# Optimization experiments

Measured on AMD Instinct MI355X. Metric: run time of the kernel, lower is better.

Reference implementation:

```python
import jax, jax.numpy as jnp
import numpy as np

H = 16
D = 64
EPS = 1e-6

def _phi(x):
    # elu_feature_map: elu(x) + 1
    return jax.nn.elu(x) + 1.0

def setup_inputs() -> dict:
    key = jax.random.key(0)
    k1, k2, k3, k4 = jax.random.split(key, 4)
    B, N = 4, 4096
    query = jax.random.normal(k1, (B, N, H * D), dtype=jnp.float32)
    key_t = jax.random.normal(k2, (B, N, H * D), dtype=jnp.float32)
    value = jax.random.normal(k3, (B, N, H * D), dtype=jnp.float32)
    W_out = jax.random.normal(k4, (D, H * D), dtype=jnp.float32) * (1.0 / np.sqrt(H * D))
    b_out = jnp.zeros((D,), dtype=jnp.float32)
    return {"query": query, "key": key_t, "value": value, "W_out": W_out, "b_out": b_out}

def reference(query, key, value, W_out, b_out):
    B, N, _ = query.shape
    # b n (h d) -> b h n d
    def split_heads(x):
        return x.reshape(B, N, H, D).transpose(0, 2, 1, 3)
    q = split_heads(query)
    k = split_heads(key)
    v = split_heads(value)
    Q = _phi(q)  # [B,H,N,D]
    K = _phi(k)
    # KV aggregation: O(N D^2)
    KV = jnp.einsum('bhnd,bhnm->bhdm', K, v)          # [B,H,D,D]
    Ksum = K.sum(axis=2)                               # [B,H,D]
    Z = 1.0 / (jnp.einsum('bhnd,bhd->bhn', Q, Ksum) + EPS)  # [B,H,N]
    out = jnp.einsum('bhnd,bhdm,bhn->bhnm', Q, KV, Z)  # [B,H,N,D]
    # b h n d -> b n h d -> (b*n, h*d)
    out = out.transpose(0, 2, 1, 3).reshape(B * N, H * D)
    return out @ W_out.T + b_out
```

## Files before the change

### kernel.cpp

```cpp
#include <hip/hip_runtime.h>

#define B_  4
#define N_  4096
#define H_  16
#define BH_ 64
#define S_  16
#define ST_ 72
#define EPS_ 1e-6f

#define NST_ 40
#define WTILE_ (64 * NST_)
#define WPOOL_ (2 * WTILE_)

typedef _Float16 h2  __attribute__((ext_vector_type(2)));
typedef _Float16 h8  __attribute__((ext_vector_type(8)));
typedef float    f4v __attribute__((ext_vector_type(4)));

struct H2x2 { h2 a, b; };
struct H2x4 { h2 e[4]; };

__device__ __forceinline__ h8 ld_h8(const _Float16* p) {
    f4v r = *(const f4v*)p;
    return __builtin_bit_cast(h8, r);
}
__device__ __forceinline__ H2x4 ld_h2x4(const _Float16* p) {
    f4v r = *(const f4v*)p;
    return __builtin_bit_cast(H2x4, r);
}
__device__ __forceinline__ void st_h2x2(_Float16* p, h2 a, h2 b) {
    H2x2 t{a, b};
    *(float2*)p = __builtin_bit_cast(float2, t);
}
__device__ __forceinline__ float phi(float x) {
    return x > 0.0f ? x + 1.0f : __expf(x);
}
__device__ __forceinline__ float fdot2(h2 a, h2 b, float c) {
    return __builtin_amdgcn_fdot2(a, b, c, false);
}
__device__ __forceinline__ f4v gload(const void* p) {
    f4v r;
    asm volatile("global_load_dwordx4 %0, %1, off"
                 : "=v"(r) : "v"(p) : "memory");
    return r;
}
#define VMW(N)                                                    \
    do {                                                          \
        asm volatile("s_waitcnt vmcnt(" #N ")" ::: "memory");     \
        __builtin_amdgcn_sched_barrier(0);                        \
    } while (0)

__global__ __launch_bounds__(256, 2) void k_kvpart(const float* __restrict__ K,
                                                   const float* __restrict__ V,
                                                   float* __restrict__ kvpart,
                                                   float* __restrict__ kspart) {
    const int s = blockIdx.x, h4 = blockIdx.y, b = blockIdx.z;
    const int t = threadIdx.x, wv = t >> 6, lane = t & 63;
    const int rp = lane >> 4, c4 = lane & 15;
    const int h = h4 * 4 + wv;

    __shared__ __align__(16) _Float16 pool[4 * WPOOL_];

    _Float16* Kt = pool + wv * WPOOL_;
    _Float16* Vt = Kt + WTILE_;

    f4v kr[8], vr[8];
    const float* baseK = K + ((size_t)(b * N_ + s * 256) * 1024 + h * 64 + c4 * 4);
    const float* baseV = V + ((size_t)(b * N_ + s * 256) * 1024 + h * 64 + c4 * 4);

    auto LOADX = [&](int chunk) {
        const int ro = (chunk * 32 + 8 * rp) * 1024;
        const float* gk = baseK + ro;
        const float* gv = baseV + ro;
#pragma unroll
        for (int r = 0; r < 8; ++r) kr[r] = gload(gk + r * 1024);
#pragma unroll
        for (int r = 0; r < 8; ++r) vr[r] = gload(gv + r * 1024);
    };
    auto STOREX = [&]() {
        const int nn = 8 * rp;
#pragma unroll
        for (int dj = 0; dj < 4; ++dj) {
            const int d = 4 * c4 + dj;
            h2 lo, hi;
            lo.x = (_Float16)phi(kr[0][dj]); lo.y = (_Float16)phi(kr[1][dj]);
            hi.x = (_Float16)phi(kr[2][dj]); hi.y = (_Float16)phi(kr[3][dj]);
            st_h2x2(&Kt[d * NST_ + nn], lo, hi);
            lo.x = (_Float16)phi(kr[4][dj]); lo.y = (_Float16)phi(kr[5][dj]);
            hi.x = (_Float16)phi(kr[6][dj]); hi.y = (_Float16)phi(kr[7][dj]);
            st_h2x2(&Kt[d * NST_ + nn + 4], lo, hi);
            lo.x = (_Float16)vr[0][dj]; lo.y = (_Float16)vr[1][dj];
            hi.x = (_Float16)vr[2][dj]; hi.y = (_Float16)vr[3][dj];
            st_h2x2(&Vt[d * NST_ + nn], lo, hi);
            lo.x = (_Float16)vr[4][dj]; lo.y = (_Float16)vr[5][dj];
            hi.x = (_Float16)vr[6][dj]; hi.y = (_Float16)vr[7][dj];
            st_h2x2(&Vt[d * NST_ + nn + 4], lo, hi);
        }
    };

    f4v acc[4][4];
#pragma unroll
    for (int i = 0; i < 4; ++i)
#pragma unroll
        for (int j = 0; j < 4; ++j) acc[i][j] = (f4v){0.f, 0.f, 0.f, 0.f};
    float ksum = 0.f;
    h2 one2; one2.x = (_Float16)1.0f; one2.y = (_Float16)1.0f;

    const int fo = rp * 8;

    auto COMPUTE = [&]() {
        h8 af[4], bf[4];
#pragma unroll
        for (int i = 0; i < 4; ++i) {
            af[i] = ld_h8(&Kt[(16 * i + c4) * NST_ + fo]);
            bf[i] = ld_h8(&Vt[(16 * i + c4) * NST_ + fo]);
        }
#pragma unroll
        for (int i = 0; i < 4; ++i)
#pragma unroll
            for (int j = 0; j < 4; ++j)
                acc[i][j] = __builtin_amdgcn_mfma_f32_16x16x32_f16(af[i], bf[j], acc[i][j], 0, 0, 0);
#pragma unroll
        for (int q = 0; q < 4; ++q) {
            H2x4 x = ld_h2x4(&Kt[lane * NST_ + q * 8]);
#pragma unroll
            for (int i = 0; i < 4; ++i) ksum = fdot2(x.e[i], one2, ksum);
        }
    };

    LOADX(0);
    VMW(0);
    STOREX();
#pragma unroll
    for (int c = 0; c < 8; ++c) {
        if (c < 7) LOADX(c + 1);
        COMPUTE();
        if (c < 7) {
            VMW(0);
            STOREX();
        }
    }

    const int bh = b * 16 + h;
    float* outp = kvpart + (size_t)(bh * S_ + s) * 4096;
#pragma unroll
    for (int i = 0; i < 4; ++i)
#pragma unroll
        for (int j = 0; j < 4; ++j)
#pragma unroll
            for (int r = 0; r < 4; ++r) {
                const int d = 16 * i + rp * 4 + r;
                const int m = 16 * j + c4;
                outp[d * 64 + m] = acc[i][j][r];
            }
    kspart[(size_t)(bh * S_ + s) * 64 + lane] = ksum;
}

__global__ __launch_bounds__(256, 2) void k_makeM(const float* __restrict__ kvpart,
                                                  const float* __restrict__ kspart,
                                                  const float* __restrict__ W,
                                                  _Float16* __restrict__ Mt,
                                                  float* __restrict__ Ksum) {
    const int bh = blockIdx.x, dq = blockIdx.y;
    const int h  = bh & 15;
    const int t  = threadIdx.x;

    __shared__ float KVs[16][68];
    __shared__ float Ws[64][68];

    const f4v* W4  = (const f4v*)W;

    f4v rr[S_];
    {
        const int row = t >> 4, c4 = t & 15;
        const float* g = kvpart + ((size_t)(bh * S_) * 4096 +
                                   (dq * 16 + row) * 64 + c4 * 4);
#pragma unroll
        for (int s = 0; s < S_; ++s) rr[s] = gload(g + (size_t)s * 4096);
    }
    for (int idx = t; idx < 1024; idx += 256) {
        int wrow = idx >> 4, wc = idx & 15;
        *(f4v*)&Ws[wrow][wc * 4] = W4[(size_t)wrow * 256 + h * 16 + wc];
    }
    if (dq == 0 && t < 64) {
        float ks = 0.f;
#pragma unroll
        for (int s = 0; s < S_; ++s) ks += kspart[(size_t)(bh * S_ + s) * 64 + t];
        Ksum[(size_t)bh * 64 + t] = ks;
    }
    VMW(0);
    {
        const int row = t >> 4, c4 = t & 15;
        f4v r = {0.f, 0.f, 0.f, 0.f};
#pragma unroll
        for (int s = 0; s < S_; ++s) r += rr[s];
        *(f4v*)&KVs[row][c4 * 4] = r;
    }
    __syncthreads();

    const int j = t >> 2, dl = (t & 3) * 4;
    float acc[4] = {0.f, 0.f, 0.f, 0.f};
#pragma unroll 4
    for (int m4 = 0; m4 < 16; ++m4) {
        f4v wr  = *(const f4v*)&Ws[j][m4 * 4];
        f4v kv0 = *(const f4v*)&KVs[dl + 0][m4 * 4];
        f4v kv1 = *(const f4v*)&KVs[dl + 1][m4 * 4];
        f4v kv2 = *(const f4v*)&KVs[dl + 2][m4 * 4];
        f4v kv3 = *(const f4v*)&KVs[dl + 3][m4 * 4];
        acc[0] += wr[0] * kv0[0] + wr[1] * kv0[1] + wr[2] * kv0[2] + wr[3] * kv0[3];
        acc[1] += wr[0] * kv1[0] + wr[1] * kv1[1] + wr[2] * kv1[2] + wr[3] * kv1[3];
        acc[2] += wr[0] * kv2[0] + wr[1] * kv2[1] + wr[2] * kv2[2] + wr[3] * kv2[3];
        acc[3] += wr[0] * kv3[0] + wr[1] * kv3[1] + wr[2] * kv3[2] + wr[3] * kv3[3];
    }
    h2 lo, hi;
    lo.x = (_Float16)acc[0]; lo.y = (_Float16)acc[1];
    hi.x = (_Float16)acc[2]; hi.y = (_Float16)acc[3];
    H2x2 pk{lo, hi};
    *(float2*)&Mt[((size_t)bh * 64 + j) * 64 + dq * 16 + dl] =
        __builtin_bit_cast(float2, pk);
}

__global__ __launch_bounds__(256, 2) void k_out(const float* __restrict__ Q,
                                                const _Float16* __restrict__ Mtg,
                                                const float* __restrict__ Ksum,
                                                const float* __restrict__ bout,
                                                float* __restrict__ out) {
    const int nc = blockIdx.x, b = blockIdx.y;
    const int n0 = nc * 64;
    const int t = threadIdx.x, w = t >> 6, lane = t & 63;
    const int rp4 = t >> 4, c4 = t & 15;

    __shared__ __align__(16) _Float16 pool[2 * 2 * 64 * ST_];
    __shared__ float zz[64];
    __shared__ h2 Kss[2][32];

    f4v qr[4], mr[2];
    float ksa = 0.f, ksb = 0.f;
    auto LOAD = [&](int hh) {
        const int bh = b * 16 + hh;
        const float* gq = Q + ((size_t)(b * N_ + n0 + rp4) * 1024 + hh * 64 + c4 * 4);
        qr[0] = gload(gq);
        qr[1] = gload(gq + 16 * 1024);
        qr[2] = gload(gq + 32 * 1024);
        qr[3] = gload(gq + 48 * 1024);
        const _Float16* gm = Mtg + ((size_t)bh * 4096 + t * 8);
        mr[0] = gload(gm);
        mr[1] = gload(gm + 2048);
        if (t < 32) {
            ksa = Ksum[(size_t)bh * 64 + 2 * t];
            ksb = Ksum[(size_t)bh * 64 + 2 * t + 1];
        }
    };
    auto STORE = [&](int buf) {
        _Float16* Qp = pool + buf * (2 * 64 * ST_);
        _Float16* Mt = Qp + 64 * ST_;
#pragma unroll
        for (int r = 0; r < 4; ++r) {
            int row = rp4 + 16 * r;
            h2 p0, p1;
            p0.x = (_Float16)phi(qr[r][0]); p0.y = (_Float16)phi(qr[r][1]);
            p1.x = (_Float16)phi(qr[r][2]); p1.y = (_Float16)phi(qr[r][3]);
            st_h2x2(&Qp[row * ST_ + 4 * c4], p0, p1);
        }
        *(f4v*)&Mt[(t >> 3) * ST_ + (t & 7) * 8] = mr[0];
        *(f4v*)&Mt[((t + 256) >> 3) * ST_ + (t & 7) * 8] = mr[1];
        if (t < 32) { h2 kk; kk.x = (_Float16)ksa; kk.y = (_Float16)ksb; Kss[buf][t] = kk; }
    };

    const int tn0 = 2 * (w >> 1), tj0 = 2 * (w & 1);
    const int rA = lane & 15, fo = (lane >> 4) * 8;
    float facc[2][2][4] = {{{0.f}}};

    LOAD(0);
    VMW(0);
    STORE(0);

    for (int hh = 0; hh < 16; ++hh) {
        if (hh + 1 < 16) LOAD(hh + 1);
        __syncthreads();
        const int buf = hh & 1;
        const _Float16* Qp = pool + buf * (2 * 64 * ST_);
        const _Float16* Mt = Qp + 64 * ST_;

        if (t < 64) {
            float zp = 0.f;
#pragma unroll
            for (int c = 0; c < 8; ++c) {
                H2x4 x = ld_h2x4(&Qp[t * ST_ + c * 8]);
#pragma unroll
                for (int i = 0; i < 4; ++i) zp = fdot2(x.e[i], Kss[buf][c * 4 + i], zp);
            }
            zz[t] = 1.0f / (zp + EPS_);
        }
        __syncthreads();

        f4v acc[2][2];
#pragma unroll
        for (int a = 0; a < 2; ++a)
#pragma unroll
            for (int bb = 0; bb < 2; ++bb) acc[a][bb] = (f4v){0.f, 0.f, 0.f, 0.f};
#pragma unroll
        for (int ks = 0; ks < 2; ++ks) {
            h8 a0 = ld_h8(&Qp[(16 * (tn0 + 0) + rA) * ST_ + ks * 32 + fo]);
            h8 a1 = ld_h8(&Qp[(16 * (tn0 + 1) + rA) * ST_ + ks * 32 + fo]);
            h8 b0 = ld_h8(&Mt[(16 * (tj0 + 0) + rA) * ST_ + ks * 32 + fo]);
            h8 b1 = ld_h8(&Mt[(16 * (tj0 + 1) + rA) * ST_ + ks * 32 + fo]);
            acc[0][0] = __builtin_amdgcn_mfma_f32_16x16x32_f16(a0, b0, acc[0][0], 0, 0, 0);
            acc[0][1] = __builtin_amdgcn_mfma_f32_16x16x32_f16(a0, b1, acc[0][1], 0, 0, 0);
            acc[1][0] = __builtin_amdgcn_mfma_f32_16x16x32_f16(a1, b0, acc[1][0], 0, 0, 0);
            acc[1][1] = __builtin_amdgcn_mfma_f32_16x16x32_f16(a1, b1, acc[1][1], 0, 0, 0);
        }
#pragma unroll
        for (int a = 0; a < 2; ++a)
#pragma unroll
            for (int r = 0; r < 4; ++r) {
                int row = 16 * (tn0 + a) + (lane >> 4) * 4 + r;
                float z = zz[row];
                facc[a][0][r] += z * acc[a][0][r];
                facc[a][1][r] += z * acc[a][1][r];
            }
        if (hh + 1 < 16) {
            VMW(0);
            STORE((hh + 1) & 1);
        }
    }

#pragma unroll
    for (int a = 0; a < 2; ++a)
#pragma unroll
        for (int bb = 0; bb < 2; ++bb) {
            const int j = 16 * (tj0 + bb) + (lane & 15);
            const float bj = bout[j];
#pragma unroll
            for (int r = 0; r < 4; ++r) {
                int n = 16 * (tn0 + a) + (lane >> 4) * 4 + r;
                out[(size_t)(b * N_ + n0 + n) * 64 + j] = bj + facc[a][bb][r];
            }
        }
}

extern "C" void kernel_launch(void* const* d_in, const int* in_sizes, int n_in,
                              void* d_out, int out_size, void* d_ws, size_t ws_size,
                              hipStream_t stream) {
    const float* q  = (const float*)d_in[0];
    const float* k  = (const float*)d_in[1];
    const float* v  = (const float*)d_in[2];
    const float* W  = (const float*)d_in[3];
    const float* bo = (const float*)d_in[4];
    float* out = (float*)d_out;

    float* ws      = (float*)d_ws;
    float* kvpart  = ws;
    float* kspart  = kvpart + (size_t)BH_ * S_ * 4096;
    float* Mt      = kspart + (size_t)BH_ * S_ * 64;
    float* Ksum    = Mt + (size_t)BH_ * 4096 / 2;

    k_kvpart<<<dim3(S_, 4, 4), 256, 0, stream>>>(k, v, kvpart, kspart);
    k_makeM<<<dim3(BH_, 4), 256, 0, stream>>>(kvpart, kspart, W, (_Float16*)Mt, Ksum);
    k_out<<<dim3(N_ / 64, B_), 256, 0, stream>>>(q, (const _Float16*)Mt, Ksum, bo, out);
}
```

Before: 226.7 us.

## Double-buffer K/V loads two chunks ahead in kvpart and use lgkm barriers

The kvpart kernel now keeps two register sets and two LDS buffers per wave, so global loads run two chunks ahead of the fp16 store and MFMA compute, with explicit vmcnt/lgkmcnt waits. This doubles LDS and register use, so launch bounds drop to one block per SIMD pair, trading occupancy for deeper prefetch. The second kernel replaces __syncthreads with an explicit lgkmcnt wait plus s_barrier, and waits for LDS before issuing the next global loads.

```diff
diff --git a/kernel.cpp b/kernel.cpp
--- a/kernel.cpp
+++ b/kernel.cpp
@@ -48,8 +48,19 @@
         asm volatile("s_waitcnt vmcnt(" #N ")" ::: "memory");     \
         __builtin_amdgcn_sched_barrier(0);                        \
     } while (0)
-
-__global__ __launch_bounds__(256, 2) void k_kvpart(const float* __restrict__ K,
+#define LGKW()                                                    \
+    do {                                                          \
+        asm volatile("s_waitcnt lgkmcnt(0)" ::: "memory");        \
+        __builtin_amdgcn_sched_barrier(0);                        \
+    } while (0)
+
+__device__ __forceinline__ void barrier_lgkm() {
+    asm volatile("s_waitcnt lgkmcnt(0)" ::: "memory");
+    __builtin_amdgcn_sched_barrier(0);
+    __builtin_amdgcn_s_barrier();
+}
+
+__global__ __launch_bounds__(256, 1) void k_kvpart(const float* __restrict__ K,
                                                    const float* __restrict__ V,
                                                    float* __restrict__ kvpart,
                                                    float* __restrict__ kspart) {
@@ -58,16 +69,13 @@
     const int rp = lane >> 4, c4 = lane & 15;
     const int h = h4 * 4 + wv;
 
-    __shared__ __align__(16) _Float16 pool[4 * WPOOL_];
-
-    _Float16* Kt = pool + wv * WPOOL_;
-    _Float16* Vt = Kt + WTILE_;
-
-    f4v kr[8], vr[8];
+    __shared__ __align__(16) _Float16 pool[8 * WPOOL_];
+
+    f4v kA[8], vA[8], kB[8], vB[8];
     const float* baseK = K + ((size_t)(b * N_ + s * 256) * 1024 + h * 64 + c4 * 4);
     const float* baseV = V + ((size_t)(b * N_ + s * 256) * 1024 + h * 64 + c4 * 4);
 
-    auto LOADX = [&](int chunk) {
+    auto LOADX = [&](f4v* kr, f4v* vr, int chunk) {
         const int ro = (chunk * 32 + 8 * rp) * 1024;
         const float* gk = baseK + ro;
         const float* gv = baseV + ro;
@@ -76,7 +84,9 @@
 #pragma unroll
         for (int r = 0; r < 8; ++r) vr[r] = gload(gv + r * 1024);
     };
-    auto STOREX = [&]() {
+    auto STOREX = [&](const f4v* kr, const f4v* vr, int bf) {
+        _Float16* Kt = pool + (wv * 2 + bf) * WPOOL_;
+        _Float16* Vt = Kt + WTILE_;
         const int nn = 8 * rp;
 #pragma unroll
         for (int dj = 0; dj < 4; ++dj) {
@@ -107,18 +117,20 @@
 
     const int fo = rp * 8;
 
-    auto COMPUTE = [&]() {
-        h8 af[4], bf[4];
+    auto COMPUTE = [&](int bf) {
+        const _Float16* Kt = pool + (wv * 2 + bf) * WPOOL_;
+        const _Float16* Vt = Kt + WTILE_;
+        h8 af[4], bfv[4];
 #pragma unroll
         for (int i = 0; i < 4; ++i) {
-            af[i] = ld_h8(&Kt[(16 * i + c4) * NST_ + fo]);
-            bf[i] = ld_h8(&Vt[(16 * i + c4) * NST_ + fo]);
+            af[i]  = ld_h8(&Kt[(16 * i + c4) * NST_ + fo]);
+            bfv[i] = ld_h8(&Vt[(16 * i + c4) * NST_ + fo]);
         }
 #pragma unroll
         for (int i = 0; i < 4; ++i)
 #pragma unroll
             for (int j = 0; j < 4; ++j)
-                acc[i][j] = __builtin_amdgcn_mfma_f32_16x16x32_f16(af[i], bf[j], acc[i][j], 0, 0, 0);
+                acc[i][j] = __builtin_amdgcn_mfma_f32_16x16x32_f16(af[i], bfv[j], acc[i][j], 0, 0, 0);
 #pragma unroll
         for (int q = 0; q < 4; ++q) {
             H2x4 x = ld_h2x4(&Kt[lane * NST_ + q * 8]);
@@ -127,18 +139,16 @@
         }
     };
 
-    LOADX(0);
-    VMW(0);
-    STOREX();
-#pragma unroll
-    for (int c = 0; c < 8; ++c) {
-        if (c < 7) LOADX(c + 1);
-        COMPUTE();
-        if (c < 7) {
-            VMW(0);
-            STOREX();
-        }
-    }
+    LOADX(kA, vA, 0);
+    LOADX(kB, vB, 1);
+    VMW(16); STOREX(kA, vA, 0); LGKW(); LOADX(kA, vA, 2); COMPUTE(0);
+    VMW(16); STOREX(kB, vB, 1); LGKW(); LOADX(kB, vB, 3); COMPUTE(1);
+    VMW(16); STOREX(kA, vA, 0); LGKW(); LOADX(kA, vA, 4); COMPUTE(0);
+    VMW(16); STOREX(kB, vB, 1); LGKW(); LOADX(kB, vB, 5); COMPUTE(1);
+    VMW(16); STOREX(kA, vA, 0); LGKW(); LOADX(kA, vA, 6); COMPUTE(0);
+    VMW(16); STOREX(kB, vB, 1); LGKW(); LOADX(kB, vB, 7); COMPUTE(1);
+    VMW(16); STOREX(kA, vA, 0); COMPUTE(0);
+    VMW(0);  STOREX(kB, vB, 1); COMPUTE(1);
 
     const int bh = b * 16 + h;
     float* outp = kvpart + (size_t)(bh * S_ + s) * 4096;
@@ -275,8 +285,8 @@
     STORE(0);
 
     for (int hh = 0; hh < 16; ++hh) {
-        if (hh + 1 < 16) LOAD(hh + 1);
-        __syncthreads();
+        if (hh + 1 < 16) { LGKW(); LOAD(hh + 1); }
+        barrier_lgkm();
         const int buf = hh & 1;
         const _Float16* Qp = pool + buf * (2 * 64 * ST_);
         const _Float16* Mt = Qp + 64 * ST_;
@@ -291,7 +301,7 @@
             }
             zz[t] = 1.0f / (zp + EPS_);
         }
-        __syncthreads();
+        barrier_lgkm();
 
         f4v acc[2][2];
 #pragma unroll
```

New measurement: 221.2 us. 2.4% less time.

## Shrink per-block tiles in kvpart and out kernels to raise block count

Applied to the files above, without the earlier changes.

k_kvpart now assigns one head per block, with the four waves splitting the D rows of that head and sharing a double-buffered LDS tile under __syncthreads. Previously each wave handled its own head with a private tile. k_out now processes 16 query rows per block instead of 64, giving four times more blocks with one MFMA tile per wave. Both kernels drop the inline-asm loads and waitcnt barriers and raise launch bounds to 4 blocks per CU. The aim is more parallelism and occupancy for latency hiding. The cost is more block-level syncs, reloading M per smaller block, and less reuse per load.

```diff
diff --git a/kernel.cpp b/kernel.cpp
--- a/kernel.cpp
+++ b/kernel.cpp
@@ -5,12 +5,11 @@
 #define H_  16
 #define BH_ 64
 #define S_  16
-#define ST_ 72
 #define EPS_ 1e-6f
 
 #define NST_ 40
-#define WTILE_ (64 * NST_)
-#define WPOOL_ (2 * WTILE_)
+#define TSZ_ 2560
+#define KOST_ 72
 
 typedef _Float16 h2  __attribute__((ext_vector_type(2)));
 typedef _Float16 h8  __attribute__((ext_vector_type(8)));
@@ -49,110 +48,93 @@
         __builtin_amdgcn_sched_barrier(0);                        \
     } while (0)
 
-__global__ __launch_bounds__(256, 2) void k_kvpart(const float* __restrict__ K,
+__global__ __launch_bounds__(256, 4) void k_kvpart(const float* __restrict__ K,
                                                    const float* __restrict__ V,
                                                    float* __restrict__ kvpart,
                                                    float* __restrict__ kspart) {
-    const int s = blockIdx.x, h4 = blockIdx.y, b = blockIdx.z;
+    const int s = blockIdx.x, h = blockIdx.y, b = blockIdx.z;
     const int t = threadIdx.x, wv = t >> 6, lane = t & 63;
-    const int rp = lane >> 4, c4 = lane & 15;
-    const int h = h4 * 4 + wv;
-
-    __shared__ __align__(16) _Float16 pool[4 * WPOOL_];
-
-    _Float16* Kt = pool + wv * WPOOL_;
-    _Float16* Vt = Kt + WTILE_;
-
-    f4v kr[8], vr[8];
+    const int rp2 = t >> 4, c4 = t & 15;
+    const int l15 = lane & 15;
+
+    __shared__ __align__(16) _Float16 pool[2 * 2 * TSZ_];
+
+    f4v k0r, k1r, v0r, v1r;
     const float* baseK = K + ((size_t)(b * N_ + s * 256) * 1024 + h * 64 + c4 * 4);
     const float* baseV = V + ((size_t)(b * N_ + s * 256) * 1024 + h * 64 + c4 * 4);
 
     auto LOADX = [&](int chunk) {
-        const int ro = (chunk * 32 + 8 * rp) * 1024;
-        const float* gk = baseK + ro;
-        const float* gv = baseV + ro;
-#pragma unroll
-        for (int r = 0; r < 8; ++r) kr[r] = gload(gk + r * 1024);
-#pragma unroll
-        for (int r = 0; r < 8; ++r) vr[r] = gload(gv + r * 1024);
-    };
-    auto STOREX = [&]() {
-        const int nn = 8 * rp;
+        const int ro = (chunk * 32 + 2 * rp2) * 1024;
+        k0r = *(const f4v*)(baseK + ro);
+        k1r = *(const f4v*)(baseK + ro + 1024);
+        v0r = *(const f4v*)(baseV + ro);
+        v1r = *(const f4v*)(baseV + ro + 1024);
+    };
+    auto STOREX = [&](int bf) {
+        _Float16* Kt = pool + bf * (2 * TSZ_);
+        _Float16* Vt = Kt + TSZ_;
+        const int nn = 2 * rp2;
 #pragma unroll
         for (int dj = 0; dj < 4; ++dj) {
             const int d = 4 * c4 + dj;
-            h2 lo, hi;
-            lo.x = (_Float16)phi(kr[0][dj]); lo.y = (_Float16)phi(kr[1][dj]);
-            hi.x = (_Float16)phi(kr[2][dj]); hi.y = (_Float16)phi(kr[3][dj]);
-            st_h2x2(&Kt[d * NST_ + nn], lo, hi);
-            lo.x = (_Float16)phi(kr[4][dj]); lo.y = (_Float16)phi(kr[5][dj]);
-            hi.x = (_Float16)phi(kr[6][dj]); hi.y = (_Float16)phi(kr[7][dj]);
-            st_h2x2(&Kt[d * NST_ + nn + 4], lo, hi);
-            lo.x = (_Float16)vr[0][dj]; lo.y = (_Float16)vr[1][dj];
-            hi.x = (_Float16)vr[2][dj]; hi.y = (_Float16)vr[3][dj];
-            st_h2x2(&Vt[d * NST_ + nn], lo, hi);
-            lo.x = (_Float16)vr[4][dj]; lo.y = (_Float16)vr[5][dj];
-            hi.x = (_Float16)vr[6][dj]; hi.y = (_Float16)vr[7][dj];
-            st_h2x2(&Vt[d * NST_ + nn + 4], lo, hi);
-        }
-    };
-
-    f4v acc[4][4];
-#pragma unroll
-    for (int i = 0; i < 4; ++i)
-#pragma unroll
-        for (int j = 0; j < 4; ++j) acc[i][j] = (f4v){0.f, 0.f, 0.f, 0.f};
+            h2 kk, vv;
+            kk.x = (_Float16)phi(k0r[dj]); kk.y = (_Float16)phi(k1r[dj]);
+            vv.x = (_Float16)v0r[dj];      vv.y = (_Float16)v1r[dj];
+            *(h2*)&Kt[d * NST_ + nn] = kk;
+            *(h2*)&Vt[d * NST_ + nn] = vv;
+        }
+    };
+
+    f4v acc[4];
+#pragma unroll
+    for (int j = 0; j < 4; ++j) acc[j] = (f4v){0.f, 0.f, 0.f, 0.f};
     float ksum = 0.f;
     h2 one2; one2.x = (_Float16)1.0f; one2.y = (_Float16)1.0f;
-
-    const int fo = rp * 8;
-
-    auto COMPUTE = [&]() {
-        h8 af[4], bf[4];
-#pragma unroll
-        for (int i = 0; i < 4; ++i) {
-            af[i] = ld_h8(&Kt[(16 * i + c4) * NST_ + fo]);
-            bf[i] = ld_h8(&Vt[(16 * i + c4) * NST_ + fo]);
-        }
-#pragma unroll
-        for (int i = 0; i < 4; ++i)
-#pragma unroll
-            for (int j = 0; j < 4; ++j)
-                acc[i][j] = __builtin_amdgcn_mfma_f32_16x16x32_f16(af[i], bf[j], acc[i][j], 0, 0, 0);
-#pragma unroll
-        for (int q = 0; q < 4; ++q) {
-            H2x4 x = ld_h2x4(&Kt[lane * NST_ + q * 8]);
-#pragma unroll
-            for (int i = 0; i < 4; ++i) ksum = fdot2(x.e[i], one2, ksum);
+    const int fo = (lane >> 4) * 8;
+
+    auto COMPUTE = [&](int bf) {
+        const _Float16* Kt = pool + bf * (2 * TSZ_);
+        const _Float16* Vt = Kt + TSZ_;
+        h8 a0 = ld_h8(&Kt[(16 * wv + l15) * NST_ + fo]);
+#pragma unroll
+        for (int j = 0; j < 4; ++j) {
+            h8 b0 = ld_h8(&Vt[(16 * j + l15) * NST_ + fo]);
+            acc[j] = __builtin_amdgcn_mfma_f32_16x16x32_f16(a0, b0, acc[j], 0, 0, 0);
+        }
+        if (wv == 0) {
+#pragma unroll
+            for (int q = 0; q < 4; ++q) {
+                H2x4 x = ld_h2x4(&Kt[lane * NST_ + q * 8]);
+#pragma unroll
+                for (int i = 0; i < 4; ++i) ksum = fdot2(x.e[i], one2, ksum);
+            }
         }
     };
 
     LOADX(0);
-    VMW(0);
-    STOREX();
+    STOREX(0);
+    __syncthreads();
 #pragma unroll
     for (int c = 0; c < 8; ++c) {
         if (c < 7) LOADX(c + 1);
-        COMPUTE();
+        COMPUTE(c & 1);
         if (c < 7) {
-            VMW(0);
-            STOREX();
+            STOREX((c + 1) & 1);
+            __syncthreads();
         }
     }
 
     const int bh = b * 16 + h;
     float* outp = kvpart + (size_t)(bh * S_ + s) * 4096;
 #pragma unroll
-    for (int i = 0; i < 4; ++i)
-#pragma unroll
-        for (int j = 0; j < 4; ++j)
-#pragma unroll
-            for (int r = 0; r < 4; ++r) {
-                const int d = 16 * i + rp * 4 + r;
-                const int m = 16 * j + c4;
-                outp[d * 64 + m] = acc[i][j][r];
-            }
-    kspart[(size_t)(bh * S_ + s) * 64 + lane] = ksum;
+    for (int j = 0; j < 4; ++j)
+#pragma unroll
+        for (int r = 0; r < 4; ++r) {
+            const int d = 16 * wv + (lane >> 4) * 4 + r;
+            const int m = 16 * j + l15;
+            outp[d * 64 + m] = acc[j][r];
+        }
+    if (wv == 0) kspart[(size_t)(bh * S_ + s) * 64 + lane] = ksum;
 }
 
 __global__ __launch_bounds__(256, 2) void k_makeM(const float* __restrict__ kvpart,
@@ -219,123 +201,92 @@
         __builtin_bit_cast(float2, pk);
 }
 
-__global__ __launch_bounds__(256, 2) void k_out(const float* __restrict__ Q,
+__global__ __launch_bounds__(256, 4) void k_out(const float* __restrict__ Q,
                                                 const _Float16* __restrict__ Mtg,
                                                 const float* __restrict__ Ksum,
                                                 const float* __restrict__ bout,
                                                 float* __restrict__ out) {
     const int nc = blockIdx.x, b = blockIdx.y;
-    const int n0 = nc * 64;
-    const int t = threadIdx.x, w = t >> 6, lane = t & 63;
-    const int rp4 = t >> 4, c4 = t & 15;
-
-    __shared__ __align__(16) _Float16 pool[2 * 2 * 64 * ST_];
-    __shared__ float zz[64];
+    const int n0 = nc * 16;
+    const int t = threadIdx.x, wv = t >> 6, lane = t & 63;
+    const int rp16 = t >> 4, c4 = t & 15, l15 = lane & 15;
+
+    __shared__ __align__(16) _Float16 pool[2 * 80 * KOST_];
+    __shared__ float zz[16];
     __shared__ h2 Kss[2][32];
 
-    f4v qr[4], mr[2];
+    f4v qr, mr0, mr1;
     float ksa = 0.f, ksb = 0.f;
     auto LOAD = [&](int hh) {
         const int bh = b * 16 + hh;
-        const float* gq = Q + ((size_t)(b * N_ + n0 + rp4) * 1024 + hh * 64 + c4 * 4);
-        qr[0] = gload(gq);
-        qr[1] = gload(gq + 16 * 1024);
-        qr[2] = gload(gq + 32 * 1024);
-        qr[3] = gload(gq + 48 * 1024);
-        const _Float16* gm = Mtg + ((size_t)bh * 4096 + t * 8);
-        mr[0] = gload(gm);
-        mr[1] = gload(gm + 2048);
+        qr = *(const f4v*)(Q + ((size_t)(b * N_ + n0 + rp16) * 1024 + hh * 64 + c4 * 4));
+        const f4v* gm = (const f4v*)(Mtg + (size_t)bh * 4096);
+        mr0 = gm[t];
+        mr1 = gm[t + 256];
         if (t < 32) {
             ksa = Ksum[(size_t)bh * 64 + 2 * t];
             ksb = Ksum[(size_t)bh * 64 + 2 * t + 1];
         }
     };
-    auto STORE = [&](int buf) {
-        _Float16* Qp = pool + buf * (2 * 64 * ST_);
-        _Float16* Mt = Qp + 64 * ST_;
-#pragma unroll
-        for (int r = 0; r < 4; ++r) {
-            int row = rp4 + 16 * r;
-            h2 p0, p1;
-            p0.x = (_Float16)phi(qr[r][0]); p0.y = (_Float16)phi(qr[r][1]);
-            p1.x = (_Float16)phi(qr[r][2]); p1.y = (_Float16)phi(qr[r][3]);
-            st_h2x2(&Qp[row * ST_ + 4 * c4], p0, p1);
-        }
-        *(f4v*)&Mt[(t >> 3) * ST_ + (t & 7) * 8] = mr[0];
-        *(f4v*)&Mt[((t + 256) >> 3) * ST_ + (t & 7) * 8] = mr[1];
-        if (t < 32) { h2 kk; kk.x = (_Float16)ksa; kk.y = (_Float16)ksb; Kss[buf][t] = kk; }
-    };
-
-    const int tn0 = 2 * (w >> 1), tj0 = 2 * (w & 1);
-    const int rA = lane & 15, fo = (lane >> 4) * 8;
-    float facc[2][2][4] = {{{0.f}}};
+    auto STORE = [&](int bf) {
+        _Float16* Qp = pool + bf * (80 * KOST_);
+        _Float16* Mt = Qp + 16 * KOST_;
+        h2 p0, p1;
+        p0.x = (_Float16)phi(qr[0]); p0.y = (_Float16)phi(qr[1]);
+        p1.x = (_Float16)phi(qr[2]); p1.y = (_Float16)phi(qr[3]);
+        st_h2x2(&Qp[rp16 * KOST_ + 4 * c4], p0, p1);
+        *(f4v*)&Mt[(t >> 3) * KOST_ + (t & 7) * 8] = mr0;
+        *(f4v*)&Mt[((t + 256) >> 3) * KOST_ + (t & 7) * 8] = mr1;
+        if (t < 32) { h2 kk; kk.x = (_Float16)ksa; kk.y = (_Float16)ksb; Kss[bf][t] = kk; }
+    };
+
+    const int fo = (lane >> 4) * 8;
+    float facc[4] = {0.f, 0.f, 0.f, 0.f};
 
     LOAD(0);
-    VMW(0);
     STORE(0);
 
     for (int hh = 0; hh < 16; ++hh) {
         if (hh + 1 < 16) LOAD(hh + 1);
         __syncthreads();
-        const int buf = hh & 1;
-        const _Float16* Qp = pool + buf * (2 * 64 * ST_);
-        const _Float16* Mt = Qp + 64 * ST_;
-
-        if (t < 64) {
+        const int bf = hh & 1;
+        const _Float16* Qp = pool + bf * (80 * KOST_);
+        const _Float16* Mt = Qp + 16 * KOST_;
+
+        if (t < 16) {
             float zp = 0.f;
 #pragma unroll
             for (int c = 0; c < 8; ++c) {
-                H2x4 x = ld_h2x4(&Qp[t * ST_ + c * 8]);
-#pragma unroll
-                for (int i = 0; i < 4; ++i) zp = fdot2(x.e[i], Kss[buf][c * 4 + i], zp);
+                H2x4 x = ld_h2x4(&Qp[t * KOST_ + c * 8]);
+#pragma unroll
+                for (int i = 0; i < 4; ++i) zp = fdot2(x.e[i], Kss[bf][c * 4 + i], zp);
             }
             zz[t] = 1.0f / (zp + EPS_);
         }
         __syncthreads();
 
-        f4v acc[2][2];
-#pragma unroll
-        for (int a = 0; a < 2; ++a)
-#pragma unroll
-            for (int bb = 0; bb < 2; ++bb) acc[a][bb] = (f4v){0.f, 0.f, 0.f, 0.f};
+        f4v acc = (f4v){0.f, 0.f, 0.f, 0.f};
 #pragma unroll
         for (int ks = 0; ks < 2; ++ks) {
-            h8 a0 = ld_h8(&Qp[(16 * (tn0 + 0) + rA) * ST_ + ks * 32 + fo]);
-            h8 a1 = ld_h8(&Qp[(16 * (tn0 + 1) + rA) * ST_ + ks * 32 + fo]);
-            h8 b0 = ld_h8(&Mt[(16 * (tj0 + 0) + rA) * ST_ + ks * 32 + fo]);
-            h8 b1 = ld_h8(&Mt[(16 * (tj0 + 1) + rA) * ST_ + ks * 32 + fo]);
-            acc[0][0] = __builtin_amdgcn_mfma_f32_16x16x32_f16(a0, b0, acc[0][0], 0, 0, 0);
-            acc[0][1] = __builtin_amdgcn_mfma_f32_16x16x32_f16(a0, b1, acc[0][1], 0, 0, 0);
-            acc[1][0] = __builtin_amdgcn_mfma_f32_16x16x32_f16(a1, b0, acc[1][0], 0, 0, 0);
-            acc[1][1] = __builtin_amdgcn_mfma_f32_16x16x32_f16(a1, b1, acc[1][1], 0, 0, 0);
-        }
-#pragma unroll
-        for (int a = 0; a < 2; ++a)
-#pragma unroll
-            for (int r = 0; r < 4; ++r) {
-                int row = 16 * (tn0 + a) + (lane >> 4) * 4 + r;
-                float z = zz[row];
-                facc[a][0][r] += z * acc[a][0][r];
-                facc[a][1][r] += z * acc[a][1][r];
-            }
-        if (hh + 1 < 16) {
-            VMW(0);
-            STORE((hh + 1) & 1);
-        }
-    }
-
-#pragma unroll
-    for (int a = 0; a < 2; ++a)
-#pragma unroll
-        for (int bb = 0; bb < 2; ++bb) {
-            const int j = 16 * (tj0 + bb) + (lane & 15);
-            const float bj = bout[j];
-#pragma unroll
-            for (int r = 0; r < 4; ++r) {
-                int n = 16 * (tn0 + a) + (lane >> 4) * 4 + r;
-                out[(size_t)(b * N_ + n0 + n) * 64 + j] = bj + facc[a][bb][r];
-            }
-        }
+            h8 a0 = ld_h8(&Qp[l15 * KOST_ + ks * 32 + fo]);
+            h8 b0 = ld_h8(&Mt[(16 * wv + l15) * KOST_ + ks * 32 + fo]);
+            acc = __builtin_amdgcn_mfma_f32_16x16x32_f16(a0, b0, acc, 0, 0, 0);
+        }
+#pragma unroll
+        for (int r = 0; r < 4; ++r) {
+            const int row = (lane >> 4) * 4 + r;
+            facc[r] += zz[row] * acc[r];
+        }
+        if (hh + 1 < 16) STORE((hh + 1) & 1);
+    }
+
+    const int j = 16 * wv + l15;
+    const float bj = bout[j];
+#pragma unroll
+    for (int r = 0; r < 4; ++r) {
+        const int n = n0 + (lane >> 4) * 4 + r;
+        out[(size_t)(b * N_ + n) * 64 + j] = bj + facc[r];
+    }
 }
 
 extern "C" void kernel_launch(void* const* d_in, const int* in_sizes, int n_in,
@@ -354,7 +305,7 @@
     float* Mt      = kspart + (size_t)BH_ * S_ * 64;
     float* Ksum    = Mt + (size_t)BH_ * 4096 / 2;
 
-    k_kvpart<<<dim3(S_, 4, 4), 256, 0, stream>>>(k, v, kvpart, kspart);
+    k_kvpart<<<dim3(S_, H_, B_), 256, 0, stream>>>(k, v, kvpart, kspart);
     k_makeM<<<dim3(BH_, 4), 256, 0, stream>>>(kvpart, kspart, W, (_Float16*)Mt, Ksum);
-    k_out<<<dim3(N_ / 64, B_), 256, 0, stream>>>(q, (const _Float16*)Mt, Ksum, bo, out);
-}
+    k_out<<<dim3(N_ / 16, B_), 256, 0, stream>>>(q, (const _Float16*)Mt, Ksum, bo, out);
+}
```

After: 222.9 us. No clear change (-1.7%).
